# Performance work log

Measured on AMD Instinct MI355X. Metric: run time of the kernel, lower is better.

## Reference

```python
import math
import jax, jax.numpy as jnp
import numpy as np

B, H, T, NH, D = 2, 4, 2048, 8192, 256
THETA = 65536.0  # rope_theta = 2**16
TWO_PI = 2.0 * math.pi


def get_freqs(n, theta):
    # quantize(arange(n), q=2) = floor(i/2)*2, so dim pairs share a frequency
    idx = jnp.arange(n, dtype=jnp.float32)
    q = jnp.floor(idx / 2.0) * 2.0
    return 1.0 / (theta ** (q / n)) / TWO_PI


def rope(phases, v):
    ph = (phases % 1.0) * TWO_PI
    c = jnp.cos(ph)
    s = jnp.sin(ph)
    # interleaved pair rotation: (-v1, v0, -v3, v2, ...)
    v_rot = jnp.stack((-v[..., 1::2], v[..., ::2]), axis=-1).reshape(v.shape)
    return v * c + v_rot * s


def setup_inputs() -> dict:
    key = jax.random.key(0)
    k1, k2, k3 = jax.random.split(key, 3)
    Q = jax.random.normal(k1, (B, H, T, NH), dtype=jnp.float32)
    K = jax.random.normal(k2, (B, H, T, NH), dtype=jnp.float32)
    V = jax.random.normal(k3, (B, 1, T, D), dtype=jnp.float32)
    return {"Q": Q, "K": K, "V": V}


def reference(Q, K, V):
    freqs = get_freqs(NH, THETA).reshape(1, 1, 1, NH)          # [1,1,1,NH]
    t = jnp.arange(T, dtype=jnp.float32).reshape(1, 1, T, 1)    # [1,1,T,1]
    phases = t * freqs                                          # [1,1,T,NH]
    Qr = rope(phases, Q)
    Kr = rope(phases, K)
    scores = jnp.einsum('bhtn,bhsn->bhts', Qr, Kr)              # [B,H,T,T]
    mask = jnp.tril(jnp.ones((T, T), dtype=bool), k=-1)         # strictly lower
    scores = jnp.where(mask, scores, jnp.float32(0.0))
    # V: [B,1,T,D] broadcasts over heads
    return jnp.matmul(scores, V)                                # [B,H,T,D]
```

## Files before the change

kernel.cpp:

```cpp
#include <hip/hip_runtime.h>
#include <hip/hip_bf16.h>

#define B_ 2
#define H_ 4
#define T_ 2048
#define NH_ 8192
#define D_ 256

typedef __attribute__((ext_vector_type(4))) float f32x4;
typedef __attribute__((ext_vector_type(8))) short bf16x8;
typedef __attribute__((ext_vector_type(4))) int i32x4;

__device__ __forceinline__ unsigned short f2bf(float f) {
    union { float f; unsigned u; } v;
    v.f = f;
    unsigned u = v.u;
    unsigned r = u + 0x7FFFu + ((u >> 16) & 1u);
    return (unsigned short)(r >> 16);
}

__global__ __launch_bounds__(256) void rope_cast_kernel(
    const float* __restrict__ Q, const float* __restrict__ K,
    unsigned short* __restrict__ Qb, unsigned short* __restrict__ Kb,
    int bh0)
{
    const long gid = (long)blockIdx.x * 256 + threadIdx.x;
    const int ng = NH_ / 8;
    const int n8 = (int)(gid % ng) * 8;
    const long row = gid / ng;
    const int t = (int)(row % T_);
    const int lbh = (int)(row / T_);

    const long in_off  = ((long)(bh0 + lbh) * T_ + t) * NH_ + n8;
    const long out_off = ((long)lbh * T_ + t) * NH_ + n8;

    float4 qa = *(const float4*)(Q + in_off);
    float4 qb4 = *(const float4*)(Q + in_off + 4);
    float4 ka = *(const float4*)(K + in_off);
    float4 kb4 = *(const float4*)(K + in_off + 4);
    float qv[8] = {qa.x, qa.y, qa.z, qa.w, qb4.x, qb4.y, qb4.z, qb4.w};
    float kv[8] = {ka.x, ka.y, ka.z, ka.w, kb4.x, kb4.y, kb4.z, kb4.w};

    union { i32x4 v; unsigned short u[8]; } qo, ko;
    const int p0 = n8 >> 1;
    const float tf = (float)t;
#pragma unroll
    for (int j = 0; j < 4; ++j) {
        float freq = exp2f(-(float)(p0 + j) * (1.0f / 256.0f)) * 0.15915494309189535f;
        float phase = tf * freq;
        float r = phase - floorf(phase);
        float c, s;
        asm("v_cos_f32 %0, %1" : "=v"(c) : "v"(r));
        asm("v_sin_f32 %0, %1" : "=v"(s) : "v"(r));
        float qe = qv[2 * j], qodd = qv[2 * j + 1];
        float ke = kv[2 * j], kodd = kv[2 * j + 1];
        qo.u[2 * j]     = f2bf(qe * c - qodd * s);
        qo.u[2 * j + 1] = f2bf(qodd * c + qe * s);
        ko.u[2 * j]     = f2bf(ke * c - kodd * s);
        ko.u[2 * j + 1] = f2bf(kodd * c + ke * s);
    }
    *(i32x4*)(Qb + out_off) = qo.v;
    *(i32x4*)(Kb + out_off) = ko.v;
}

__global__ __launch_bounds__(256) void vcast_kernel(
    const float* __restrict__ V, unsigned short* __restrict__ Vt)
{
    __shared__ unsigned short tile[64][72];
    const int t0 = blockIdx.x * 64;
    const int d0 = blockIdx.y * 64;
    const int b = blockIdx.z;
    const int tid = threadIdx.x;
#pragma unroll
    for (int rr = 0; rr < 16; ++rr) {
        int tl = rr * 4 + (tid >> 6);
        int dl = tid & 63;
        float v = V[((long)b * T_ + (t0 + tl)) * D_ + d0 + dl];
        tile[dl][tl] = f2bf(v);
    }
    __syncthreads();
#pragma unroll
    for (int rr = 0; rr < 16; ++rr) {
        int dl = rr * 4 + (tid >> 6);
        int tl = tid & 63;
        Vt[((long)b * D_ + (d0 + dl)) * T_ + t0 + tl] = tile[dl][tl];
    }
}

#define GLD16(g, l) __builtin_amdgcn_global_load_lds(                         \
    (const __attribute__((address_space(1))) void*)(g),                       \
    (__attribute__((address_space(3))) void*)(l), 16, 0, 0)

__global__ __launch_bounds__(512, 2) void gemm1_kernel(
    const unsigned short* __restrict__ Qb, const unsigned short* __restrict__ Kb,
    unsigned short* __restrict__ S, float* __restrict__ part, int split)
{
    __shared__ __align__(16) unsigned short As[3][256][32];
    __shared__ __align__(16) unsigned short Bs[3][256][32];

    const int bidx = blockIdx.x;
    int lbh, t36, KT, kc, pidx;
    bool full;
    if (split) {
        lbh = bidx & 7;
        const int s = bidx >> 3;
        if (s < 32) { t36 = s; KT = 256; kc = 0; full = true; pidx = 0; }
        else {
            const int j = s - 32;
            t36 = 32 + (j >> 3);
            kc = j & 7;
            KT = 32; full = false;
            pidx = (lbh * 4 + (t36 - 32)) * 8 + kc;
        }
    } else {
        lbh = bidx / 36; t36 = bidx % 36; KT = 256; kc = 0; full = true; pidx = 0;
    }
    int it = (int)((sqrtf(8.0f * (float)t36 + 1.0f) - 1.0f) * 0.5f);
    if ((it + 1) * (it + 2) / 2 <= t36) ++it;
    if (it * (it + 1) / 2 > t36) --it;
    const int jt = t36 - it * (it + 1) / 2;

    const int tid = threadIdx.x;
    const int lane = tid & 63;
    const int wid = tid >> 6;
    const int wr = wid >> 2;
    const int wc = wid & 3;
    const int rofs = lane & 15;
    const int sl8 = (((lane >> 4) ^ ((lane >> 1) & 3))) << 3;

    const int ss8 = (((tid & 3) ^ ((tid >> 3) & 3))) << 3;
    const int dst = tid * 8;
    const long K0 = (long)kc * 1024;
    const unsigned short* Ab = Qb + (long)lbh * T_ * NH_ + (long)it * 256 * NH_ + K0;
    const unsigned short* Bb = Kb + (long)lbh * T_ * NH_ + (long)jt * 256 * NH_ + K0;
    const unsigned short* gA0 = Ab + (long)(tid >> 2) * NH_ + ss8;
    const unsigned short* gA1 = gA0 + 128L * NH_;
    const unsigned short* gB0 = Bb + (long)(tid >> 2) * NH_ + ss8;
    const unsigned short* gB1 = gB0 + 128L * NH_;
    unsigned short* AsB = &As[0][0][0];
    unsigned short* BsB = &Bs[0][0][0];

    f32x4 acc[8][4];
#pragma unroll
    for (int m = 0; m < 8; ++m)
#pragma unroll
        for (int n = 0; n < 4; ++n)
            acc[m][n] = (f32x4){0.f, 0.f, 0.f, 0.f};

#define G256_STAGE(SB, kt) {                                                  \
    const long ko_ = (long)(kt) * 32;                                         \
    GLD16(gA0 + ko_, AsB + (SB) * 8192 + dst);                                \
    GLD16(gA1 + ko_, AsB + (SB) * 8192 + 4096 + dst);                         \
    GLD16(gB0 + ko_, BsB + (SB) * 8192 + dst);                                \
    GLD16(gB1 + ko_, BsB + (SB) * 8192 + 4096 + dst); }

    G256_STAGE(0, 0)
    G256_STAGE(1, 1)
    asm volatile("s_waitcnt vmcnt(4)" ::: "memory");
    __builtin_amdgcn_s_barrier();
    __builtin_amdgcn_sched_barrier(0);

    const int arow = wr * 128 + rofs;
    const int brow = wc * 64 + rofs;
#pragma unroll 1
    for (int t = 0; t < KT; ++t) {
        const int rb = t % 3;
        bf16x8 af[8], bv[4];
        const unsigned short* ab = AsB + rb * 8192 + sl8;
        const unsigned short* bb = BsB + rb * 8192 + sl8;
#pragma unroll
        for (int n = 0; n < 4; ++n)
            bv[n] = *(const bf16x8*)(bb + (brow + n * 16) * 32);
#pragma unroll
        for (int m = 0; m < 8; ++m)
            af[m] = *(const bf16x8*)(ab + (arow + m * 16) * 32);
        if (t + 2 < KT) { const int sb = (t + 2) % 3; G256_STAGE(sb, t + 2) }
        __builtin_amdgcn_s_setprio(1);
#pragma unroll
        for (int m = 0; m < 8; ++m)
#pragma unroll
            for (int n = 0; n < 4; ++n)
                acc[m][n] = __builtin_amdgcn_mfma_f32_16x16x32_bf16(
                    af[m], bv[n], acc[m][n], 0, 0, 0);
        __builtin_amdgcn_s_setprio(0);
        if (t < KT - 2) {
            asm volatile("s_waitcnt vmcnt(4)" ::: "memory");
            __builtin_amdgcn_s_barrier();
            __builtin_amdgcn_sched_barrier(0);
        } else if (t == KT - 2) {
            asm volatile("s_waitcnt vmcnt(0)" ::: "memory");
            __builtin_amdgcn_s_barrier();
            __builtin_amdgcn_sched_barrier(0);
        }
    }

    if (full) {
        unsigned short* Sp = S + (long)lbh * T_ * T_;
        const int r0 = it * 256 + wr * 128 + ((lane >> 4) << 2);
        const int c0 = jt * 256 + wc * 64 + (lane & 15);
#pragma unroll
        for (int m = 0; m < 8; ++m) {
#pragma unroll
            for (int i = 0; i < 4; ++i) {
                const int rr = r0 + m * 16 + i;
#pragma unroll
                for (int n = 0; n < 4; ++n) {
                    const int cc = c0 + n * 16;
                    float v = (cc < rr) ? acc[m][n][i] : 0.0f;
                    Sp[(long)rr * T_ + cc] = f2bf(v);
                }
            }
        }
    } else {
        float* Pp = part + (long)pidx * 65536;
        const int r0 = wr * 128 + ((lane >> 4) << 2);
        const int c0 = wc * 64 + (lane & 15);
#pragma unroll
        for (int m = 0; m < 8; ++m) {
#pragma unroll
            for (int i = 0; i < 4; ++i) {
                const int rr = r0 + m * 16 + i;
#pragma unroll
                for (int n = 0; n < 4; ++n)
                    Pp[rr * 256 + c0 + n * 16] = acc[m][n][i];
            }
        }
    }
#undef G256_STAGE
}

__global__ __launch_bounds__(256) void reduce_kernel(
    const float* __restrict__ part, unsigned short* __restrict__ S)
{
    const int b = blockIdx.x;
    const int q = b >> 6;
    const int e0 = (b & 63) * 1024 + threadIdx.x * 4;
    const int lbh = q >> 2;
    const int jt = 4 + (q & 3);
    const int it = 7;

    float4 s = {0.f, 0.f, 0.f, 0.f};
#pragma unroll
    for (int kc = 0; kc < 8; ++kc) {
        float4 p = *(const float4*)(part + ((long)(q * 8 + kc)) * 65536 + e0);
        s.x += p.x; s.y += p.y; s.z += p.z; s.w += p.w;
    }
    const int row = e0 >> 8;
    const int col = e0 & 255;
    const int rr = it * 256 + row;
    const int c0 = jt * 256 + col;
    unsigned short o[4];
#pragma unroll
    for (int k = 0; k < 4; ++k) {
        float v = ((c0 + k) < rr) ? ((const float*)&s)[k] : 0.0f;
        o[k] = f2bf(v);
    }
    unsigned short* Sp = S + (long)lbh * T_ * T_ + (long)rr * T_ + c0;
    Sp[0] = o[0]; Sp[1] = o[1]; Sp[2] = o[2]; Sp[3] = o[3];
}

__device__ __forceinline__ void stage_tile(const unsigned short* g, long ldk,
                                           unsigned short* l, int tid)
{
    const int row = tid >> 2;
    const int col = (tid & 3) << 3;
    const unsigned short* g0 = g + (long)row * ldk + col;
    const unsigned short* g1 = g0 + 64 * ldk;
    unsigned short* l0 = l + tid * 8;
    unsigned short* l1 = l0 + 2048;
    GLD16(g0, l0);
    GLD16(g1, l1);
}

__global__ __launch_bounds__(256) void gemm2_kernel(
    const unsigned short* __restrict__ S, const unsigned short* __restrict__ Vt,
    float* __restrict__ Out, int bh0)
{
    const int jn = blockIdx.x;
    const int it = blockIdx.y;
    const int lbh = blockIdx.z;
    const int bh = bh0 + lbh;
    const int b = bh / H_;

    __shared__ __align__(16) unsigned short As2[2][128][32];
    __shared__ __align__(16) unsigned short Bs2[2][128][32];

    const unsigned short* A  = S + (long)lbh * T_ * T_ + (long)it * 128 * T_;
    const unsigned short* Bm = Vt + (long)b * D_ * T_ + (long)jn * 128 * T_;
    const int KT = (it + 1) * 4;

    const int tid = threadIdx.x;
    const int lane = tid & 63;
    const int wid = tid >> 6;
    const int wr = wid >> 1;
    const int wc = wid & 1;
    f32x4 acc[4][4];
#pragma unroll
    for (int m = 0; m < 4; ++m)
#pragma unroll
        for (int n = 0; n < 4; ++n)
            acc[m][n] = (f32x4){0.f, 0.f, 0.f, 0.f};
    const int rofs = lane & 15;
    const int kofs = (lane >> 4) * 8;
    stage_tile(A, T_, &As2[0][0][0], tid);
    stage_tile(Bm, T_, &Bs2[0][0][0], tid);
    int cur = 0;
    for (int kt = 0; kt < KT; ++kt) {
        __syncthreads();
        if (kt + 1 < KT) {
            stage_tile(A + (long)(kt + 1) * 32, T_, &As2[cur ^ 1][0][0], tid);
            stage_tile(Bm + (long)(kt + 1) * 32, T_, &Bs2[cur ^ 1][0][0], tid);
        }
        bf16x8 af[4], bfr[4];
#pragma unroll
        for (int m = 0; m < 4; ++m)
            af[m] = *(const bf16x8*)&As2[cur][wr * 64 + m * 16 + rofs][kofs];
#pragma unroll
        for (int n = 0; n < 4; ++n)
            bfr[n] = *(const bf16x8*)&Bs2[cur][wc * 64 + n * 16 + rofs][kofs];
#pragma unroll
        for (int m = 0; m < 4; ++m)
#pragma unroll
            for (int n = 0; n < 4; ++n)
                acc[m][n] = __builtin_amdgcn_mfma_f32_16x16x32_bf16(
                    af[m], bfr[n], acc[m][n], 0, 0, 0);
        cur ^= 1;
    }

    float* Op = Out + ((long)bh * T_ + it * 128) * D_ + jn * 128;
#pragma unroll
    for (int m = 0; m < 4; ++m) {
        const int rbase = wr * 64 + m * 16 + ((lane >> 4) << 2);
#pragma unroll
        for (int i = 0; i < 4; ++i) {
            const int rr = rbase + i;
#pragma unroll
            for (int n = 0; n < 4; ++n) {
                const int cc = wc * 64 + n * 16 + (lane & 15);
                Op[(long)rr * D_ + cc] = acc[m][n][i];
            }
        }
    }
}

extern "C" void kernel_launch(void* const* d_in, const int* in_sizes, int n_in,
                              void* d_out, int out_size, void* d_ws, size_t ws_size,
                              hipStream_t stream)
{
    const float* Q = (const float*)d_in[0];
    const float* K = (const float*)d_in[1];
    const float* V = (const float*)d_in[2];
    float* Out = (float*)d_out;

    const size_t vt_elems = (size_t)B_ * D_ * T_;
    const size_t part_bytes = 256ull * 65536ull * 4ull;
    auto need = [&](int c, bool split) {
        return 2 * vt_elems + (size_t)c * T_ * NH_ * 2 * 2
             + (size_t)c * T_ * T_ * 2
             + (split ? part_bytes : 0);
    };
    int c; bool split;
    if      (ws_size >= need(8, true))  { c = 8; split = true; }
    else if (ws_size >= need(8, false)) { c = 8; split = false; }
    else if (ws_size >= need(4, false)) { c = 4; split = false; }
    else if (ws_size >= need(2, false)) { c = 2; split = false; }
    else if (ws_size >= need(1, false)) { c = 1; split = false; }
    else return;

    unsigned short* Vt = (unsigned short*)d_ws;
    unsigned short* Qb = Vt + vt_elems;
    unsigned short* Kb = Qb + (size_t)c * T_ * NH_;
    unsigned short* Sb = Kb + (size_t)c * T_ * NH_;
    float* part = (float*)(Sb + (size_t)c * T_ * T_);

    vcast_kernel<<<dim3(T_ / 64, D_ / 64, B_), 256, 0, stream>>>(V, Vt);

    for (int bh0 = 0; bh0 < B_ * H_; bh0 += c) {
        const long groups = (long)c * T_ * (NH_ / 8);
        rope_cast_kernel<<<(int)(groups / 256), 256, 0, stream>>>(Q, K, Qb, Kb, bh0);
        if (split) {
            gemm1_kernel<<<dim3(512), 512, 0, stream>>>(Qb, Kb, Sb, part, 1);
            reduce_kernel<<<dim3(32 * 64), 256, 0, stream>>>(part, Sb);
        } else {
            gemm1_kernel<<<dim3(36 * c), 512, 0, stream>>>(Qb, Kb, Sb, part, 0);
        }
        gemm2_kernel<<<dim3(2, 16, c), 256, 0, stream>>>(Sb, Vt, Out, bh0);
    }
}
```

Measured before the change: 667.8 us.

## Replace direct-to-LDS triple buffering with register-staged double buffering in gemm1

The QK^T GEMM kernel no longer loads global tiles straight into shared memory through three LDS buffers. Each thread now loads its slice of the next tile into registers, runs the MFMA step on the current buffer, then writes those registers into the other of two LDS buffers before a barrier. The aim is to cut the LDS footprint from three stages to two and to hide global latency behind the MFMA work. The cost is about 32 extra VGPRs per thread on top of a large accumulator under a 512x2 launch bound, which risks spills or lower occupancy. Moving data through registers also adds VALU and LDS-write instructions that global_load_lds avoided.

```diff
diff --git a/kernel.cpp b/kernel.cpp
--- a/kernel.cpp
+++ b/kernel.cpp
@@ -95,8 +95,8 @@
     const unsigned short* __restrict__ Qb, const unsigned short* __restrict__ Kb,
     unsigned short* __restrict__ S, float* __restrict__ part, int split)
 {
-    __shared__ __align__(16) unsigned short As[3][256][32];
-    __shared__ __align__(16) unsigned short Bs[3][256][32];
+    __shared__ __align__(16) unsigned short As[2][256][32];
+    __shared__ __align__(16) unsigned short Bs[2][256][32];
 
     const int bidx = blockIdx.x;
     int lbh, t36, KT, kc, pidx;
@@ -147,52 +147,65 @@
         for (int n = 0; n < 4; ++n)
             acc[m][n] = (f32x4){0.f, 0.f, 0.f, 0.f};
 
-#define G256_STAGE(SB, kt) {                                                  \
-    const long ko_ = (long)(kt) * 32;                                         \
-    GLD16(gA0 + ko_, AsB + (SB) * 8192 + dst);                                \
-    GLD16(gA1 + ko_, AsB + (SB) * 8192 + 4096 + dst);                         \
-    GLD16(gB0 + ko_, BsB + (SB) * 8192 + dst);                                \
-    GLD16(gB1 + ko_, BsB + (SB) * 8192 + 4096 + dst); }
-
-    G256_STAGE(0, 0)
-    G256_STAGE(1, 1)
-    asm volatile("s_waitcnt vmcnt(4)" ::: "memory");
-    __builtin_amdgcn_s_barrier();
-    __builtin_amdgcn_sched_barrier(0);
+    i32x4 xa0, xa1, xb0, xb1;
+    i32x4 ya0, ya1, yb0, yb1;
+
+#define LDX(kt) { const long ko_ = (long)(kt) * 32;                           \
+    xa0 = *(const i32x4*)(gA0 + ko_); xa1 = *(const i32x4*)(gA1 + ko_);       \
+    xb0 = *(const i32x4*)(gB0 + ko_); xb1 = *(const i32x4*)(gB1 + ko_); }
+#define LDY(kt) { const long ko_ = (long)(kt) * 32;                           \
+    ya0 = *(const i32x4*)(gA0 + ko_); ya1 = *(const i32x4*)(gA1 + ko_);       \
+    yb0 = *(const i32x4*)(gB0 + ko_); yb1 = *(const i32x4*)(gB1 + ko_); }
+#define WRX(P) {                                                              \
+    *(i32x4*)(AsB + (P) * 8192 + dst) = xa0;                                  \
+    *(i32x4*)(AsB + (P) * 8192 + 4096 + dst) = xa1;                           \
+    *(i32x4*)(BsB + (P) * 8192 + dst) = xb0;                                  \
+    *(i32x4*)(BsB + (P) * 8192 + 4096 + dst) = xb1; }
+#define WRY(P) {                                                              \
+    *(i32x4*)(AsB + (P) * 8192 + dst) = ya0;                                  \
+    *(i32x4*)(AsB + (P) * 8192 + 4096 + dst) = ya1;                           \
+    *(i32x4*)(BsB + (P) * 8192 + dst) = yb0;                                  \
+    *(i32x4*)(BsB + (P) * 8192 + 4096 + dst) = yb1; }
+#define BARR { asm volatile("s_waitcnt lgkmcnt(0)" ::: "memory");             \
+    __builtin_amdgcn_s_barrier();                                             \
+    __builtin_amdgcn_sched_barrier(0); }
+#define MM(P) { bf16x8 af[8], bv[4];                                          \
+    const unsigned short* ab = AsB + (P) * 8192 + sl8;                        \
+    const unsigned short* bb = BsB + (P) * 8192 + sl8;                        \
+    _Pragma("unroll") for (int n = 0; n < 4; ++n)                             \
+        bv[n] = *(const bf16x8*)(bb + (brow + n * 16) * 32);                  \
+    _Pragma("unroll") for (int m = 0; m < 8; ++m)                             \
+        af[m] = *(const bf16x8*)(ab + (arow + m * 16) * 32);                  \
+    __builtin_amdgcn_s_setprio(1);                                            \
+    _Pragma("unroll") for (int m = 0; m < 8; ++m)                             \
+        _Pragma("unroll") for (int n = 0; n < 4; ++n)                         \
+            acc[m][n] = __builtin_amdgcn_mfma_f32_16x16x32_bf16(              \
+                af[m], bv[n], acc[m][n], 0, 0, 0);                            \
+    __builtin_amdgcn_s_setprio(0); }
 
     const int arow = wr * 128 + rofs;
     const int brow = wc * 64 + rofs;
+
+    LDX(0)
+    LDY(1)
+    WRX(0)
+    BARR
+
 #pragma unroll 1
-    for (int t = 0; t < KT; ++t) {
-        const int rb = t % 3;
-        bf16x8 af[8], bv[4];
-        const unsigned short* ab = AsB + rb * 8192 + sl8;
-        const unsigned short* bb = BsB + rb * 8192 + sl8;
-#pragma unroll
-        for (int n = 0; n < 4; ++n)
-            bv[n] = *(const bf16x8*)(bb + (brow + n * 16) * 32);
-#pragma unroll
-        for (int m = 0; m < 8; ++m)
-            af[m] = *(const bf16x8*)(ab + (arow + m * 16) * 32);
-        if (t + 2 < KT) { const int sb = (t + 2) % 3; G256_STAGE(sb, t + 2) }
-        __builtin_amdgcn_s_setprio(1);
-#pragma unroll
-        for (int m = 0; m < 8; ++m)
-#pragma unroll
-            for (int n = 0; n < 4; ++n)
-                acc[m][n] = __builtin_amdgcn_mfma_f32_16x16x32_bf16(
-                    af[m], bv[n], acc[m][n], 0, 0, 0);
-        __builtin_amdgcn_s_setprio(0);
-        if (t < KT - 2) {
-            asm volatile("s_waitcnt vmcnt(4)" ::: "memory");
-            __builtin_amdgcn_s_barrier();
-            __builtin_amdgcn_sched_barrier(0);
-        } else if (t == KT - 2) {
-            asm volatile("s_waitcnt vmcnt(0)" ::: "memory");
-            __builtin_amdgcn_s_barrier();
-            __builtin_amdgcn_sched_barrier(0);
-        }
-    }
+    for (int t = 0; t + 2 < KT; t += 2) {
+        LDX(t + 2)
+        MM(0)
+        WRY(1)
+        BARR
+        if (t + 3 < KT) LDY(t + 3)
+        MM(1)
+        WRX(0)
+        BARR
+    }
+    MM(0)
+    WRY(1)
+    BARR
+    MM(1)
 
     if (full) {
         unsigned short* Sp = S + (long)lbh * T_ * T_;
@@ -226,7 +239,12 @@
             }
         }
     }
-#undef G256_STAGE
+#undef LDX
+#undef LDY
+#undef WRX
+#undef WRY
+#undef BARR
+#undef MM
 }
 
 __global__ __launch_bounds__(256) void reduce_kernel(
```

New measurement: 662.0 us, median of 2. About the same (-0.9%).
